# Kernel tuning notes

Hardware: AMD Instinct MI355X
Metric: run time of the kernel (lower is better)

Reference implementation:

```python
import jax, jax.numpy as jnp
import numpy as np

HID = 1024
HEADS = 16

def setup_inputs() -> dict:
    key = jax.random.key(0)
    ks = jax.random.split(key, 9)
    s = 1.0 / np.sqrt(HID)
    x = jax.random.normal(ks[0], (4, 2048, HID), dtype=jnp.float32)
    Wq = jax.random.normal(ks[1], (HID, HID), dtype=jnp.float32) * s
    bq = jnp.zeros((HID,), dtype=jnp.float32)
    Wk = jax.random.normal(ks[2], (HID, HID), dtype=jnp.float32) * s
    bk = jnp.zeros((HID,), dtype=jnp.float32)
    Wv = jax.random.normal(ks[3], (HID, HID), dtype=jnp.float32) * s
    bv = jnp.zeros((HID,), dtype=jnp.float32)
    Wo = jax.random.normal(ks[4], (HID, HID), dtype=jnp.float32) * s
    bo = jnp.zeros((HID,), dtype=jnp.float32)
    return {"x": x, "Wq": Wq, "bq": bq, "Wk": Wk, "bk": bk,
            "Wv": Wv, "bv": bv, "Wo": Wo, "bo": bo}

def _split_heads(t):  # [b, n, hid] -> [b, h, n, d]
    b, n, _ = t.shape
    return t.reshape(b, n, HEADS, HID // HEADS).transpose(0, 2, 1, 3)

def reference(x, Wq, bq, Wk, bk, Wv, bv, Wo, bo):
    # nn.Linear: y = x @ W.T + b
    q = _split_heads(x @ Wq.T + bq)
    k = _split_heads(x @ Wk.T + bk)
    v = _split_heads(x @ Wv.T + bv)
    energy = jnp.einsum('bhqd,bhkd->bhqk', q, k)
    scaling = HID ** 0.5  # note: sqrt(hid_channels), NOT sqrt(head_dim)
    att = jax.nn.softmax(energy / scaling, axis=-1)
    out = jnp.einsum('bhqk,bhkd->bhqd', att, v)
    b, h, n, d = out.shape
    out = out.transpose(0, 2, 1, 3).reshape(b, n, h * d)
    return out @ Wo.T + bo
```

## Files before the change

kernel.cpp:

```cpp
#include <hip/hip_runtime.h>
#include <stdint.h>


#define HID 1024
#define NH 16
#define HD 64
#define BB 4
#define SEQ 2048
#define MTOT (BB * SEQ)

typedef short bf16x8 __attribute__((ext_vector_type(8)));
typedef float f32x4 __attribute__((ext_vector_type(4)));

#define SWZ(row, cb) ((cb) ^ (((row) & 7) << 4))

#define GLDS(gp, lp) __builtin_amdgcn_global_load_lds( \
    (const __attribute__((address_space(1))) void*)(gp), \
    (__attribute__((address_space(3))) void*)(lp), 16, 0, 0)

static __device__ __forceinline__ unsigned short f2bf(float f) {
  unsigned u = __float_as_uint(f);
  u += 0x7fffu + ((u >> 16) & 1u);
  return (unsigned short)(u >> 16);
}

static __device__ __forceinline__ f32x4 mfma16(bf16x8 a, bf16x8 b, f32x4 c) {
  return __builtin_amdgcn_mfma_f32_16x16x32_bf16(a, b, c, 0, 0, 0);
}

__global__ void k_cvt_all(const float* __restrict__ x,
                          const float* __restrict__ Wq, const float* __restrict__ Wk,
                          const float* __restrict__ Wv, const float* __restrict__ Wo,
                          unsigned short* __restrict__ ws) {
  const int X4 = MTOT * HID / 4;
  const int W4 = HID * HID / 4;
  int i = blockIdx.x * blockDim.x + threadIdx.x;
  const float* src;
  unsigned short* dst;
  int off;
  if (i < X4) {
    src = x; dst = ws; off = i;
  } else {
    int j = i - X4;
    int w = j / W4;
    off = j - w * W4;
    src = (w == 0) ? Wq : (w == 1) ? Wk : (w == 2) ? Wv : Wo;
    dst = ws + (size_t)MTOT * HID + (size_t)w * HID * HID;
  }
  float4 v = reinterpret_cast<const float4*>(src)[off];
  ushort4 o;
  o.x = f2bf(v.x); o.y = f2bf(v.y); o.z = f2bf(v.z); o.w = f2bf(v.w);
  reinterpret_cast<ushort4*>(dst)[off] = o;
}

__global__ __launch_bounds__(256, 2) void k_gemm3(
    const unsigned short* __restrict__ A,
    const unsigned short* __restrict__ W3,
    const float* __restrict__ bq, const float* __restrict__ bk,
    const float* __restrict__ bv,
    unsigned short* __restrict__ Qo,
    unsigned short* __restrict__ Ko,
    unsigned short* __restrict__ Vto,
    float cexp) {
  const int K = HID;
  __shared__ __align__(16) unsigned short sA[128 * 64];
  __shared__ __align__(16) unsigned short sB[128 * 64];
  const int orig = blockIdx.x + gridDim.x * blockIdx.y;
  const int xcd = orig & 7, idx = orig >> 3;
  const int gm = xcd & 3, gn = xcd >> 1 >> 1;
  const int m0 = (gm * 16 + (idx & 15)) * 128;
  const int n0 = (gn * 12 + (idx >> 4)) * 128;
  const int tid = threadIdx.x;
  const int lane = tid & 63, wid = tid >> 6;
  const int wr = wid >> 1, wc = wid & 1;
  const int lr = lane & 15, lg = lane >> 4;

  f32x4 acc[4][4] = {};

  const unsigned short* gA = A + (size_t)m0 * K;
  const unsigned short* gW = W3 + (size_t)n0 * K;

  for (int kt = 0; kt < K; kt += 64) {
#pragma unroll
    for (int i = 0; i < 4; ++i) {
      int c = tid + i * 256;
      int row = c >> 3, col = (c & 7) << 3;
      GLDS(gA + (size_t)row * K + kt + col, (char*)sA + (size_t)c * 16);
      GLDS(gW + (size_t)row * K + kt + col, (char*)sB + (size_t)c * 16);
    }
    __syncthreads();
#pragma unroll
    for (int kk = 0; kk < 64; kk += 32) {
      bf16x8 a[4], b[4];
      const int co = kk + lg * 8;
#pragma unroll
      for (int m = 0; m < 4; ++m)
        a[m] = *reinterpret_cast<const bf16x8*>(sA + (wr * 64 + m * 16 + lr) * 64 + co);
#pragma unroll
      for (int n = 0; n < 4; ++n)
        b[n] = *reinterpret_cast<const bf16x8*>(sB + (wc * 64 + n * 16 + lr) * 64 + co);
      __builtin_amdgcn_s_setprio(1);
#pragma unroll
      for (int m = 0; m < 4; ++m)
#pragma unroll
        for (int n = 0; n < 4; ++n)
          acc[m][n] = mfma16(a[m], b[n], acc[m][n]);
      __builtin_amdgcn_s_setprio(0);
    }
    __syncthreads();
  }

  const int sect = n0 >> 10;
  const float* bias = (sect == 0) ? bq : (sect == 1) ? bk : bv;
  const float sc = (sect == 0) ? cexp : 1.0f;

  if (sect < 2) {
    unsigned short* C = (sect == 0) ? Qo : Ko;
#pragma unroll
    for (int m = 0; m < 4; ++m) {
      int row0 = m0 + wr * 64 + m * 16 + lg * 4;
      int b = row0 >> 11;
#pragma unroll
      for (int n = 0; n < 4; ++n) {
        int colq = (n0 + wc * 64 + n * 16 + lr) & 1023;
        float bvv = bias[colq];
        int h = colq >> 6, d = colq & 63;
        size_t base = ((size_t)(b * NH + h) * SEQ) * HD + d;
#pragma unroll
        for (int r = 0; r < 4; ++r) {
          int tok = (row0 + r) & 2047;
          C[base + (size_t)tok * HD] = f2bf((acc[m][n][r] + bvv) * sc);
        }
      }
    }
  } else {
#pragma unroll
    for (int m = 0; m < 4; ++m) {
      int row0 = m0 + wr * 64 + m * 16 + lg * 4;
      int b = row0 >> 11;
      int tok0 = row0 & 2047;
#pragma unroll
      for (int n = 0; n < 4; ++n) {
        int colq = (n0 + wc * 64 + n * 16 + lr) & 1023;
        float bvv = bias[colq];
        int h = colq >> 6, d = colq & 63;
        ushort4 pk;
        pk.x = f2bf(acc[m][n][0] + bvv);
        pk.y = f2bf(acc[m][n][1] + bvv);
        pk.z = f2bf(acc[m][n][2] + bvv);
        pk.w = f2bf(acc[m][n][3] + bvv);
        *reinterpret_cast<ushort4*>(&Vto[((size_t)(b * NH + h) * HD + d) * SEQ + tok0]) = pk;
      }
    }
  }
}

__global__ __launch_bounds__(256, 2) void k_gemmo(
    const unsigned short* __restrict__ A,
    const unsigned short* __restrict__ W,
    const float* __restrict__ bias,
    float* __restrict__ C) {
  const int K = HID;
  __shared__ __align__(16) unsigned short sA[128 * 64];
  __shared__ __align__(16) unsigned short sB[128 * 64];
  const int orig = blockIdx.x + gridDim.x * blockIdx.y;
  const int xcd = orig & 7, idx = orig >> 3;
  const int gm = xcd & 3, gn = xcd >> 2;
  const int m0 = (gm * 16 + (idx & 15)) * 128;
  const int n0 = (gn * 4 + (idx >> 4)) * 128;
  const int tid = threadIdx.x;
  const int lane = tid & 63, wid = tid >> 6;
  const int wr = wid >> 1, wc = wid & 1;
  const int lr = lane & 15, lg = lane >> 4;

  f32x4 acc[4][4] = {};

  const unsigned short* gA = A + (size_t)m0 * K;
  const unsigned short* gW = W + (size_t)n0 * K;

  for (int kt = 0; kt < K; kt += 64) {
#pragma unroll
    for (int i = 0; i < 4; ++i) {
      int c = tid + i * 256;
      int row = c >> 3, col = (c & 7) << 3;
      GLDS(gA + (size_t)row * K + kt + col, (char*)sA + (size_t)c * 16);
      GLDS(gW + (size_t)row * K + kt + col, (char*)sB + (size_t)c * 16);
    }
    __syncthreads();
#pragma unroll
    for (int kk = 0; kk < 64; kk += 32) {
      bf16x8 a[4], b[4];
      const int co = kk + lg * 8;
#pragma unroll
      for (int m = 0; m < 4; ++m)
        a[m] = *reinterpret_cast<const bf16x8*>(sA + (wr * 64 + m * 16 + lr) * 64 + co);
#pragma unroll
      for (int n = 0; n < 4; ++n)
        b[n] = *reinterpret_cast<const bf16x8*>(sB + (wc * 64 + n * 16 + lr) * 64 + co);
      __builtin_amdgcn_s_setprio(1);
#pragma unroll
      for (int m = 0; m < 4; ++m)
#pragma unroll
        for (int n = 0; n < 4; ++n)
          acc[m][n] = mfma16(a[m], b[n], acc[m][n]);
      __builtin_amdgcn_s_setprio(0);
    }
    __syncthreads();
  }

#pragma unroll
  for (int m = 0; m < 4; ++m) {
    int row0 = m0 + wr * 64 + m * 16 + lg * 4;
#pragma unroll
    for (int n = 0; n < 4; ++n) {
      int col = n0 + wc * 64 + n * 16 + lr;
      float bvv = bias[col];
#pragma unroll
      for (int r = 0; r < 4; ++r)
        C[(size_t)(row0 + r) * HID + col] = acc[m][n][r] + bvv;
    }
  }
}

#define KVB 64

__global__ __launch_bounds__(256, 4) void k_attn(
    const unsigned short* __restrict__ Qg,
    const unsigned short* __restrict__ Kg,
    const unsigned short* __restrict__ Vt,
    unsigned short* __restrict__ Og) {
  __shared__ __align__(16) unsigned short sP[128 * 64];
  __shared__ __align__(16) unsigned short sK[KVB * 64];
  __shared__ __align__(16) unsigned short sV[KVB * 64];

  const int bh = blockIdx.x;
  const int qt = blockIdx.y;
  const int tid = threadIdx.x;
  const int lane = tid & 63, wid = tid >> 6;
  const int lr = lane & 15, lg = lane >> 4;

  const unsigned short* Qh = Qg + ((size_t)bh * SEQ + (size_t)qt * 128) * HD;
  const unsigned short* Kh = Kg + (size_t)bh * SEQ * HD;
  const unsigned short* Vh = Vt + (size_t)bh * HD * SEQ;

  const int r0 = tid >> 3, r1 = r0 + 32;
  const int cb0 = SWZ(r0, (tid & 7) << 4) >> 1;
  const int cb1 = SWZ(r1, (tid & 7) << 4) >> 1;

#pragma unroll
  for (int i = 0; i < 4; ++i) {
    int c = tid + i * 256;
    int row = c >> 3;
    int cbl = SWZ(row, (c & 7) << 4);
    GLDS(Qh + (size_t)row * HD + (cbl >> 1), (char*)sP + (size_t)c * 16);
  }
  __syncthreads();
  bf16x8 qb[2][2];
#pragma unroll
  for (int m = 0; m < 2; ++m)
#pragma unroll
    for (int kd = 0; kd < 2; ++kd) {
      int row = wid * 32 + m * 16 + lr;
      qb[m][kd] = *reinterpret_cast<const bf16x8*>(
          (const char*)sP + row * 128 + SWZ(lr, kd * 64 + lg * 16));
    }

  const unsigned short onev = (unsigned short)0x3F80;
  const bf16x8 ones = {(short)onev, (short)onev, (short)onev, (short)onev,
                       (short)onev, (short)onev, (short)onev, (short)onev};

  f32x4 acco[2][4] = {};
  f32x4 accd[2] = {};

  for (int kt = 0; kt < SEQ; kt += KVB) {
    GLDS(Kh + (size_t)(kt + r0) * HD + cb0, (char*)sK + (size_t)tid * 16);
    GLDS(Kh + (size_t)(kt + r1) * HD + cb1, (char*)sK + (size_t)(tid + 256) * 16);
    GLDS(Vh + (size_t)r0 * SEQ + kt + cb0, (char*)sV + (size_t)tid * 16);
    GLDS(Vh + (size_t)r1 * SEQ + kt + cb1, (char*)sV + (size_t)(tid + 256) * 16);
    __syncthreads();

    f32x4 accs[2][4] = {};
#pragma unroll
    for (int kd = 0; kd < 2; ++kd) {
      bf16x8 ka[4];
#pragma unroll
      for (int n = 0; n < 4; ++n)
        ka[n] = *reinterpret_cast<const bf16x8*>(
            (const char*)sK + (n * 16 + lr) * 128 + SWZ(lr, kd * 64 + lg * 16));
      __builtin_amdgcn_s_setprio(1);
#pragma unroll
      for (int n = 0; n < 4; ++n) {
        accs[0][n] = mfma16(ka[n], qb[0][kd], accs[0][n]);
        accs[1][n] = mfma16(ka[n], qb[1][kd], accs[1][n]);
      }
      __builtin_amdgcn_s_setprio(0);
    }

#pragma unroll
    for (int m = 0; m < 2; ++m) {
      const int q = wid * 32 + m * 16 + lr;
#pragma unroll
      for (int n = 0; n < 4; ++n) {
        float p0 = exp2f(accs[m][n][0]);
        float p1 = exp2f(accs[m][n][1]);
        float p2 = exp2f(accs[m][n][2]);
        float p3 = exp2f(accs[m][n][3]);
        unsigned w0, w1;
        asm("v_cvt_pk_bf16_f32 %0, %1, %2" : "=v"(w0) : "v"(p0), "v"(p1));
        asm("v_cvt_pk_bf16_f32 %0, %1, %2" : "=v"(w1) : "v"(p2), "v"(p3));
        uint2 pk; pk.x = w0; pk.y = w1;
        *reinterpret_cast<uint2*>((char*)sP + q * 128 + SWZ(q, n * 32 + lg * 8)) = pk;
      }
    }

#pragma unroll
    for (int js = 0; js < 2; ++js) {
      bf16x8 pa[2], vb[4];
#pragma unroll
      for (int m = 0; m < 2; ++m) {
        int row = wid * 32 + m * 16 + lr;
        pa[m] = *reinterpret_cast<const bf16x8*>(
            (const char*)sP + row * 128 + SWZ(lr, js * 64 + lg * 16));
      }
#pragma unroll
      for (int n = 0; n < 4; ++n)
        vb[n] = *reinterpret_cast<const bf16x8*>(
            (const char*)sV + (n * 16 + lr) * 128 + SWZ(lr, js * 64 + lg * 16));
      __builtin_amdgcn_s_setprio(1);
#pragma unroll
      for (int m = 0; m < 2; ++m) {
#pragma unroll
        for (int n = 0; n < 4; ++n)
          acco[m][n] = mfma16(pa[m], vb[n], acco[m][n]);
        accd[m] = mfma16(pa[m], ones, accd[m]);
      }
      __builtin_amdgcn_s_setprio(0);
    }
    __syncthreads();
  }

  const int b = bh >> 4, h = bh & 15;
#pragma unroll
  for (int m = 0; m < 2; ++m) {
    int tok0 = qt * 128 + wid * 32 + m * 16 + lg * 4;
#pragma unroll
    for (int r = 0; r < 4; ++r) {
      float rd = 1.0f / accd[m][r];
#pragma unroll
      for (int n = 0; n < 4; ++n) {
        int col = h * 64 + n * 16 + lr;
        Og[(size_t)(b * SEQ + tok0 + r) * HID + col] = f2bf(acco[m][n][r] * rd);
      }
    }
  }
}

extern "C" void kernel_launch(void* const* d_in, const int* in_sizes, int n_in,
                              void* d_out, int out_size, void* d_ws, size_t ws_size,
                              hipStream_t stream) {
  (void)in_sizes; (void)n_in; (void)out_size; (void)ws_size;
  const float* x = (const float*)d_in[0];
  const float* Wq = (const float*)d_in[1];
  const float* bq = (const float*)d_in[2];
  const float* Wk = (const float*)d_in[3];
  const float* bk = (const float*)d_in[4];
  const float* Wv = (const float*)d_in[5];
  const float* bv = (const float*)d_in[6];
  const float* Wo = (const float*)d_in[7];
  const float* bo = (const float*)d_in[8];

  unsigned short* ws = (unsigned short*)d_ws;
  unsigned short* xb = ws;
  unsigned short* wqb = xb + (size_t)MTOT * HID;
  unsigned short* wob = wqb + 3 * (size_t)HID * HID;
  unsigned short* qb = wob + (size_t)HID * HID;
  unsigned short* kb = qb + (size_t)MTOT * HID;
  unsigned short* vtb = kb + (size_t)MTOT * HID;
  unsigned short* ob = vtb + (size_t)MTOT * HID;

  const float cexp = 0.04508422f;

  k_cvt_all<<<(MTOT * HID / 4 + 4 * (HID * HID / 4)) / 256, 256, 0, stream>>>(
      x, Wq, Wk, Wv, Wo, ws);

  k_gemm3<<<dim3(64, 24), 256, 0, stream>>>(
      xb, wqb, bq, bk, bv, qb, kb, vtb, cexp);

  k_attn<<<dim3(64, SEQ / 128), 256, 0, stream>>>(qb, kb, vtb, ob);

  k_gemmo<<<dim3(64, 8), 256, 0, stream>>>(ob, wob, bo, (float*)d_out);
}
```

Baseline: 211.9 us.

## Use 32x32x16 MFMA in attention and keep P in registers

Switches the attention kernel from 16x16x32 to 32x32x16 bf16 MFMA. It computes S^T so that each lane's accumulator layout matches the A-operand layout of the PV product. The exp'd probabilities are packed straight into registers instead of going through the shared-memory P buffer, and the shared-memory footprint is cut to 16KB. The aims are to remove LDS round trips for P, lower LDS usage so occupancy can rise, and use the denser MFMA shape. The trade-off is that V operand reads become split 8-byte loads, and the output stores follow the new 32x32 accumulator layout.

```diff
diff --git a/kernel.cpp b/kernel.cpp
--- a/kernel.cpp
+++ b/kernel.cpp
@@ -11,6 +11,7 @@
 
 typedef short bf16x8 __attribute__((ext_vector_type(8)));
 typedef float f32x4 __attribute__((ext_vector_type(4)));
+typedef float f32x16 __attribute__((ext_vector_type(16)));
 
 #define SWZ(row, cb) ((cb) ^ (((row) & 7) << 4))
 
@@ -26,6 +27,9 @@
 
 static __device__ __forceinline__ f32x4 mfma16(bf16x8 a, bf16x8 b, f32x4 c) {
   return __builtin_amdgcn_mfma_f32_16x16x32_bf16(a, b, c, 0, 0, 0);
+}
+static __device__ __forceinline__ f32x16 mfma32(bf16x8 a, bf16x8 b, f32x16 c) {
+  return __builtin_amdgcn_mfma_f32_32x32x16_bf16(a, b, c, 0, 0, 0);
 }
 
 __global__ void k_cvt_all(const float* __restrict__ x,
@@ -229,19 +233,20 @@
     const unsigned short* __restrict__ Kg,
     const unsigned short* __restrict__ Vt,
     unsigned short* __restrict__ Og) {
-  __shared__ __align__(16) unsigned short sP[128 * 64];
-  __shared__ __align__(16) unsigned short sK[KVB * 64];
-  __shared__ __align__(16) unsigned short sV[KVB * 64];
+  __shared__ __align__(16) unsigned short smem[128 * 64];
 
   const int bh = blockIdx.x;
   const int qt = blockIdx.y;
   const int tid = threadIdx.x;
   const int lane = tid & 63, wid = tid >> 6;
-  const int lr = lane & 15, lg = lane >> 4;
+  const int l31 = lane & 31, hi = lane >> 5;
 
   const unsigned short* Qh = Qg + ((size_t)bh * SEQ + (size_t)qt * 128) * HD;
   const unsigned short* Kh = Kg + (size_t)bh * SEQ * HD;
   const unsigned short* Vh = Vt + (size_t)bh * HD * SEQ;
+
+  char* sK = (char*)smem;
+  char* sV = (char*)smem + 8192;
 
   const int r0 = tid >> 3, r1 = r0 + 32;
   const int cb0 = SWZ(r0, (tid & 7) << 4) >> 1;
@@ -252,106 +257,96 @@
     int c = tid + i * 256;
     int row = c >> 3;
     int cbl = SWZ(row, (c & 7) << 4);
-    GLDS(Qh + (size_t)row * HD + (cbl >> 1), (char*)sP + (size_t)c * 16);
+    GLDS(Qh + (size_t)row * HD + (cbl >> 1), (char*)smem + (size_t)c * 16);
   }
   __syncthreads();
-  bf16x8 qb[2][2];
-#pragma unroll
-  for (int m = 0; m < 2; ++m)
-#pragma unroll
-    for (int kd = 0; kd < 2; ++kd) {
-      int row = wid * 32 + m * 16 + lr;
-      qb[m][kd] = *reinterpret_cast<const bf16x8*>(
-          (const char*)sP + row * 128 + SWZ(lr, kd * 64 + lg * 16));
-    }
+  bf16x8 qb[4];
+  {
+    int row = wid * 32 + l31;
+#pragma unroll
+    for (int ks = 0; ks < 4; ++ks)
+      qb[ks] = *reinterpret_cast<const bf16x8*>(
+          (const char*)smem + row * 128 + SWZ(row, ks * 32 + hi * 16));
+  }
+  __syncthreads();
 
   const unsigned short onev = (unsigned short)0x3F80;
   const bf16x8 ones = {(short)onev, (short)onev, (short)onev, (short)onev,
                        (short)onev, (short)onev, (short)onev, (short)onev};
 
-  f32x4 acco[2][4] = {};
-  f32x4 accd[2] = {};
+  f32x16 acco[2] = {};
+  f32x16 accd = {};
 
   for (int kt = 0; kt < SEQ; kt += KVB) {
-    GLDS(Kh + (size_t)(kt + r0) * HD + cb0, (char*)sK + (size_t)tid * 16);
-    GLDS(Kh + (size_t)(kt + r1) * HD + cb1, (char*)sK + (size_t)(tid + 256) * 16);
-    GLDS(Vh + (size_t)r0 * SEQ + kt + cb0, (char*)sV + (size_t)tid * 16);
-    GLDS(Vh + (size_t)r1 * SEQ + kt + cb1, (char*)sV + (size_t)(tid + 256) * 16);
-    __syncthreads();
-
-    f32x4 accs[2][4] = {};
-#pragma unroll
-    for (int kd = 0; kd < 2; ++kd) {
-      bf16x8 ka[4];
-#pragma unroll
-      for (int n = 0; n < 4; ++n)
-        ka[n] = *reinterpret_cast<const bf16x8*>(
-            (const char*)sK + (n * 16 + lr) * 128 + SWZ(lr, kd * 64 + lg * 16));
+    GLDS(Kh + (size_t)(kt + r0) * HD + cb0, sK + (size_t)tid * 16);
+    GLDS(Kh + (size_t)(kt + r1) * HD + cb1, sK + (size_t)(tid + 256) * 16);
+    GLDS(Vh + (size_t)r0 * SEQ + kt + cb0, sV + (size_t)tid * 16);
+    GLDS(Vh + (size_t)r1 * SEQ + kt + cb1, sV + (size_t)(tid + 256) * 16);
+    __syncthreads();
+
+    f32x16 accs[2] = {};
+#pragma unroll
+    for (int ks = 0; ks < 4; ++ks) {
+      bf16x8 ka0 = *reinterpret_cast<const bf16x8*>(
+          sK + (0 + l31) * 128 + SWZ(l31, ks * 32 + hi * 16));
+      bf16x8 ka1 = *reinterpret_cast<const bf16x8*>(
+          sK + (32 + l31) * 128 + SWZ(32 + l31, ks * 32 + hi * 16));
       __builtin_amdgcn_s_setprio(1);
-#pragma unroll
-      for (int n = 0; n < 4; ++n) {
-        accs[0][n] = mfma16(ka[n], qb[0][kd], accs[0][n]);
-        accs[1][n] = mfma16(ka[n], qb[1][kd], accs[1][n]);
+      accs[0] = mfma32(ka0, qb[ks], accs[0]);
+      accs[1] = mfma32(ka1, qb[ks], accs[1]);
+      __builtin_amdgcn_s_setprio(0);
+    }
+
+    bf16x8 pa[4];
+#pragma unroll
+    for (int nblk = 0; nblk < 2; ++nblk) {
+      float p[16];
+#pragma unroll
+      for (int r = 0; r < 16; ++r) p[r] = exp2f(accs[nblk][r]);
+#pragma unroll
+      for (int g = 0; g < 2; ++g) {
+        const int bs = g * 8;
+        unsigned w0, w1, w2, w3;
+        asm("v_cvt_pk_bf16_f32 %0, %1, %2" : "=v"(w0) : "v"(p[bs + 0]), "v"(p[bs + 1]));
+        asm("v_cvt_pk_bf16_f32 %0, %1, %2" : "=v"(w1) : "v"(p[bs + 2]), "v"(p[bs + 3]));
+        asm("v_cvt_pk_bf16_f32 %0, %1, %2" : "=v"(w2) : "v"(p[bs + 4]), "v"(p[bs + 5]));
+        asm("v_cvt_pk_bf16_f32 %0, %1, %2" : "=v"(w3) : "v"(p[bs + 6]), "v"(p[bs + 7]));
+        uint4 pk4; pk4.x = w0; pk4.y = w1; pk4.z = w2; pk4.w = w3;
+        pa[nblk * 2 + g] = *reinterpret_cast<bf16x8*>(&pk4);
       }
+    }
+
+#pragma unroll
+    for (int i = 0; i < 4; ++i) {
+      const int bb = i * 32 + hi * 8;
+      bf16x8 vb[2];
+#pragma unroll
+      for (int dblk = 0; dblk < 2; ++dblk) {
+        const int rsw = dblk * 32 + l31;
+        const char* rowp = sV + rsw * 128;
+        uint2 lo = *reinterpret_cast<const uint2*>(rowp + SWZ(rsw, bb));
+        uint2 hi2 = *reinterpret_cast<const uint2*>(rowp + SWZ(rsw, bb + 16));
+        uint4 q4; q4.x = lo.x; q4.y = lo.y; q4.z = hi2.x; q4.w = hi2.y;
+        vb[dblk] = *reinterpret_cast<bf16x8*>(&q4);
+      }
+      __builtin_amdgcn_s_setprio(1);
+      acco[0] = mfma32(pa[i], vb[0], acco[0]);
+      acco[1] = mfma32(pa[i], vb[1], acco[1]);
+      accd = mfma32(pa[i], ones, accd);
       __builtin_amdgcn_s_setprio(0);
     }
-
-#pragma unroll
-    for (int m = 0; m < 2; ++m) {
-      const int q = wid * 32 + m * 16 + lr;
-#pragma unroll
-      for (int n = 0; n < 4; ++n) {
-        float p0 = exp2f(accs[m][n][0]);
-        float p1 = exp2f(accs[m][n][1]);
-        float p2 = exp2f(accs[m][n][2]);
-        float p3 = exp2f(accs[m][n][3]);
-        unsigned w0, w1;
-        asm("v_cvt_pk_bf16_f32 %0, %1, %2" : "=v"(w0) : "v"(p0), "v"(p1));
-        asm("v_cvt_pk_bf16_f32 %0, %1, %2" : "=v"(w1) : "v"(p2), "v"(p3));
-        uint2 pk; pk.x = w0; pk.y = w1;
-        *reinterpret_cast<uint2*>((char*)sP + q * 128 + SWZ(q, n * 32 + lg * 8)) = pk;
-      }
-    }
-
-#pragma unroll
-    for (int js = 0; js < 2; ++js) {
-      bf16x8 pa[2], vb[4];
-#pragma unroll
-      for (int m = 0; m < 2; ++m) {
-        int row = wid * 32 + m * 16 + lr;
-        pa[m] = *reinterpret_cast<const bf16x8*>(
-            (const char*)sP + row * 128 + SWZ(lr, js * 64 + lg * 16));
-      }
-#pragma unroll
-      for (int n = 0; n < 4; ++n)
-        vb[n] = *reinterpret_cast<const bf16x8*>(
-            (const char*)sV + (n * 16 + lr) * 128 + SWZ(lr, js * 64 + lg * 16));
-      __builtin_amdgcn_s_setprio(1);
-#pragma unroll
-      for (int m = 0; m < 2; ++m) {
-#pragma unroll
-        for (int n = 0; n < 4; ++n)
-          acco[m][n] = mfma16(pa[m], vb[n], acco[m][n]);
-        accd[m] = mfma16(pa[m], ones, accd[m]);
-      }
-      __builtin_amdgcn_s_setprio(0);
-    }
     __syncthreads();
   }
 
   const int b = bh >> 4, h = bh & 15;
 #pragma unroll
-  for (int m = 0; m < 2; ++m) {
-    int tok0 = qt * 128 + wid * 32 + m * 16 + lg * 4;
-#pragma unroll
-    for (int r = 0; r < 4; ++r) {
-      float rd = 1.0f / accd[m][r];
-#pragma unroll
-      for (int n = 0; n < 4; ++n) {
-        int col = h * 64 + n * 16 + lr;
-        Og[(size_t)(b * SEQ + tok0 + r) * HID + col] = f2bf(acco[m][n][r] * rd);
-      }
-    }
+  for (int reg = 0; reg < 16; ++reg) {
+    int q = (reg & 3) + 8 * (reg >> 2) + 4 * hi;
+    int tok = qt * 128 + wid * 32 + q;
+    float rd = 1.0f / accd[reg];
+    size_t rowoff = (size_t)(b * SEQ + tok) * HID + h * 64;
+    Og[rowoff + l31] = f2bf(acco[0][reg] * rd);
+    Og[rowoff + 32 + l31] = f2bf(acco[1][reg] * rd);
   }
 }
 
```

New measurement: 211.7 us. Within noise of the previous version (-0.1%).
